# Kernel optimization log

Measured on AMD Instinct MI355X. Metric: run time of the kernel, lower is better.

## Reference

```python
import jax, jax.numpy as jnp
import numpy as np

B, D, F = 32768, 512, 512  # batch, input features, output features (num_feats)


def setup_inputs() -> dict:
    key = jax.random.key(0)
    kx, kw, ka, kb = jax.random.split(key, 4)
    x = jax.random.normal(kx, (B, D), dtype=jnp.float32)
    W = jax.random.normal(kw, (F, D), dtype=jnp.float32) / np.float32(np.sqrt(D))
    a = jax.random.normal(ka, (F,), dtype=jnp.float32)
    b = jax.random.normal(kb, (F,), dtype=jnp.float32)
    return {"x": x, "W": W, "a": a, "b": b}


def reference(x, W, a, b):
    # Vectorized form of the nested map_fn:
    # out[i, f] = tanh(b[f] + a[f] * dot(W[f, :], x[i, :]))
    z = jnp.einsum('bd,fd->bf', x, W)  # [B, F] GEMM replacing per-(sample,feature) dots
    return jnp.tanh(a * z + b)
```

## Files before the change

### kernel.cpp

```cpp
#include <hip/hip_runtime.h>
#include <hip/hip_bf16.h>
#include <math.h>


typedef short        bf16x8 __attribute__((ext_vector_type(8)));
typedef float        f32x4  __attribute__((ext_vector_type(4)));
typedef unsigned int u32x2  __attribute__((ext_vector_type(2)));

static constexpr int Mdim = 32768;
static constexpr int Kdim = 512;
static constexpr int Ndim = 512;

__device__ __forceinline__ unsigned cvt_pk_bf16(float a, float b) {
  unsigned r;
  asm("v_cvt_pk_bf16_f32 %0, %1, %2" : "=v"(r) : "v"(a), "v"(b));
  return r;
}

__device__ __forceinline__ void split4(f32x4 v, u32x2& hi, u32x2& lo) {
  unsigned h0 = cvt_pk_bf16(v[0], v[1]);
  unsigned h1 = cvt_pk_bf16(v[2], v[3]);
  float f0 = __uint_as_float(h0 << 16);
  float f1 = __uint_as_float(h0 & 0xFFFF0000u);
  float f2 = __uint_as_float(h1 << 16);
  float f3 = __uint_as_float(h1 & 0xFFFF0000u);
  lo[0] = cvt_pk_bf16(v[0] - f0, v[1] - f1);
  lo[1] = cvt_pk_bf16(v[2] - f2, v[3] - f3);
  hi[0] = h0; hi[1] = h1;
}

__device__ __forceinline__ float fast_tanh(float x) {
  float e = __expf(2.0f * x);
  return 1.0f - 2.0f * __builtin_amdgcn_rcpf(e + 1.0f);
}

__device__ __forceinline__ void glds16(const unsigned short* g, unsigned short* l) {
  __builtin_amdgcn_global_load_lds(
      (const __attribute__((address_space(1))) unsigned int*)g,
      (__attribute__((address_space(3))) unsigned int*)l, 16, 0, 0);
}

__global__ __launch_bounds__(256) void split_w(const float* __restrict__ Wm,
                                               unsigned short* __restrict__ whi,
                                               unsigned short* __restrict__ wlo) {
  const int idx = blockIdx.x * 256 + threadIdx.x;
  f32x4 v = *(const f32x4*)(Wm + (size_t)idx * 4);
  u32x2 h, l;
  split4(v, h, l);
  *(u32x2*)(whi + (size_t)idx * 4) = h;
  *(u32x2*)(wlo + (size_t)idx * 4) = l;
}

__global__ __launch_bounds__(512, 4) void gemm_ws(
    const float* __restrict__ X,
    const unsigned short* __restrict__ Whi, const unsigned short* __restrict__ Wlo,
    const float* __restrict__ avec, const float* __restrict__ bvec,
    float* __restrict__ out) {
  __shared__ unsigned short lds[4][128 * 64];

  const int bid = blockIdx.x;
  const int vid = (bid & 7) * 128 + (bid >> 3);
  const int nB  = vid & 3;
  const int mB  = vid >> 2;
  const int tid  = threadIdx.x;
  const int lane = tid & 63;
  const int wid  = tid >> 6;
  const int wm = wid >> 2, wn = wid & 3;

  f32x4 acc[4][2];
#pragma unroll
  for (int i = 0; i < 4; ++i)
#pragma unroll
    for (int j = 0; j < 2; ++j) acc[i][j] = {0.f, 0.f, 0.f, 0.f};

  const int srow  = tid >> 4;
  const int scol4 = tid & 15;
  const int kcol  = scol4 * 4;
  const int soff0 = kcol >> 3;
  const float* Xb = X + (size_t)mB * 128 * Kdim;

  const int rl = lane >> 3;
  const int ssl = (lane & 7) ^ rl;
  const int brow0 = nB * 128 + wid * 16 + rl;
  const int brow1 = brow0 + 8;
  const unsigned short* srcBhi0 = Whi + (size_t)brow0 * Kdim + ssl * 8;
  const unsigned short* srcBhi1 = Whi + (size_t)brow1 * Kdim + ssl * 8;
  const unsigned short* srcBlo0 = Wlo + (size_t)brow0 * Kdim + ssl * 8;
  const unsigned short* srcBlo1 = Wlo + (size_t)brow1 * Kdim + ssl * 8;
  unsigned short* dstB0 = &lds[0][(wid * 2 + 0) * 512];
  unsigned short* dstB1 = &lds[0][(wid * 2 + 1) * 512];
  const int planeSz = 128 * 64;

  f32x4 rA[4];
#pragma unroll
  for (int i = 0; i < 4; ++i)
    rA[i] = *(const f32x4*)(Xb + (size_t)(srow + 32 * i) * Kdim + kcol);

  for (int kt = 0; kt < Kdim / 64; ++kt) {
    const int kb = kt * 64;
    glds16(srcBhi0 + kb, dstB0 + 2 * planeSz);
    glds16(srcBhi1 + kb, dstB1 + 2 * planeSz);
    glds16(srcBlo0 + kb, dstB0 + 3 * planeSz);
    glds16(srcBlo1 + kb, dstB1 + 3 * planeSz);

#pragma unroll
    for (int i = 0; i < 4; ++i) {
      const int row = srow + 32 * i;
      const int off = row * 64 + ((soff0 ^ (row & 7)) << 3) + (kcol & 7);
      u32x2 h, l;
      split4(rA[i], h, l);
      *(u32x2*)&lds[0][off] = h;
      *(u32x2*)&lds[1][off] = l;
    }
    __syncthreads();

    if (kt != Kdim / 64 - 1) {
#pragma unroll
      for (int i = 0; i < 4; ++i)
        rA[i] = *(const f32x4*)(Xb + (size_t)(srow + 32 * i) * Kdim + kb + 64 + kcol);
    }

#pragma unroll
    for (int ks = 0; ks < 2; ++ks) {
      const int slotBase = ks * 4 + (lane >> 4);
      bf16x8 bh[2], bl[2];
#pragma unroll
      for (int ni = 0; ni < 2; ++ni) {
        const int row = wn * 32 + ni * 16 + (lane & 15);
        const int off = row * 64 + ((slotBase ^ (row & 7)) << 3);
        bh[ni] = *(const bf16x8*)&lds[2][off];
        bl[ni] = *(const bf16x8*)&lds[3][off];
      }
#pragma unroll
      for (int mi = 0; mi < 4; ++mi) {
        const int row = wm * 64 + mi * 16 + (lane & 15);
        const int off = row * 64 + ((slotBase ^ (row & 7)) << 3);
        bf16x8 ah = *(const bf16x8*)&lds[0][off];
        bf16x8 al = *(const bf16x8*)&lds[1][off];
#pragma unroll
        for (int ni = 0; ni < 2; ++ni) {
          acc[mi][ni] = __builtin_amdgcn_mfma_f32_16x16x32_bf16(ah, bh[ni], acc[mi][ni], 0, 0, 0);
          acc[mi][ni] = __builtin_amdgcn_mfma_f32_16x16x32_bf16(ah, bl[ni], acc[mi][ni], 0, 0, 0);
          acc[mi][ni] = __builtin_amdgcn_mfma_f32_16x16x32_bf16(al, bh[ni], acc[mi][ni], 0, 0, 0);
        }
      }
    }
    __syncthreads();
  }

  const int c  = lane & 15;
  const int rq = (lane >> 4) * 4;
#pragma unroll
  for (int ni = 0; ni < 2; ++ni) {
    const int gc = nB * 128 + wn * 32 + ni * 16 + c;
    const float aa = avec[gc];
    const float bb = bvec[gc];
#pragma unroll
    for (int mi = 0; mi < 4; ++mi) {
      const int gr = mB * 128 + wm * 64 + mi * 16 + rq;
      f32x4 v = acc[mi][ni];
#pragma unroll
      for (int j = 0; j < 4; ++j) {
        out[(size_t)(gr + j) * Ndim + gc] = fast_tanh(aa * v[j] + bb);
      }
    }
  }
}

__global__ __launch_bounds__(512, 4) void gemm_nows(
    const float* __restrict__ X, const float* __restrict__ Wm,
    const float* __restrict__ avec, const float* __restrict__ bvec,
    float* __restrict__ out) {
  __shared__ unsigned short lds[4][128 * 64];
  const int bid = blockIdx.x;
  const int nB  = bid & 3;
  const int mB  = bid >> 2;
  const int tid  = threadIdx.x;
  const int lane = tid & 63;
  const int wid  = tid >> 6;
  const int wm = wid >> 2, wn = wid & 3;

  f32x4 acc[4][2];
#pragma unroll
  for (int i = 0; i < 4; ++i)
#pragma unroll
    for (int j = 0; j < 2; ++j) acc[i][j] = {0.f, 0.f, 0.f, 0.f};

  const int srow  = tid >> 4;
  const int scol4 = tid & 15;
  const int kcol  = scol4 * 4;
  const int soff0 = kcol >> 3;
  const float* Xb = X  + (size_t)mB * 128 * Kdim;
  const float* Wb = Wm + (size_t)nB * 128 * Kdim;

  f32x4 rA[4], rB[4];
#pragma unroll
  for (int i = 0; i < 4; ++i) {
    const int row = srow + 32 * i;
    rA[i] = *(const f32x4*)(Xb + (size_t)row * Kdim + kcol);
    rB[i] = *(const f32x4*)(Wb + (size_t)row * Kdim + kcol);
  }

  for (int kt = 0; kt < Kdim / 64; ++kt) {
#pragma unroll
    for (int i = 0; i < 4; ++i) {
      const int row = srow + 32 * i;
      const int off = row * 64 + ((soff0 ^ (row & 7)) << 3) + (kcol & 7);
      u32x2 h, l;
      split4(rA[i], h, l);
      *(u32x2*)&lds[0][off] = h;
      *(u32x2*)&lds[1][off] = l;
      split4(rB[i], h, l);
      *(u32x2*)&lds[2][off] = h;
      *(u32x2*)&lds[3][off] = l;
    }
    __syncthreads();
    if (kt != Kdim / 64 - 1) {
      const int kbase = (kt + 1) * 64;
#pragma unroll
      for (int i = 0; i < 4; ++i) {
        const int row = srow + 32 * i;
        rA[i] = *(const f32x4*)(Xb + (size_t)row * Kdim + kbase + kcol);
        rB[i] = *(const f32x4*)(Wb + (size_t)row * Kdim + kbase + kcol);
      }
    }
#pragma unroll
    for (int ks = 0; ks < 2; ++ks) {
      const int slotBase = ks * 4 + (lane >> 4);
      bf16x8 bh[2], bl[2];
#pragma unroll
      for (int ni = 0; ni < 2; ++ni) {
        const int row = wn * 32 + ni * 16 + (lane & 15);
        const int off = row * 64 + ((slotBase ^ (row & 7)) << 3);
        bh[ni] = *(const bf16x8*)&lds[2][off];
        bl[ni] = *(const bf16x8*)&lds[3][off];
      }
#pragma unroll
      for (int mi = 0; mi < 4; ++mi) {
        const int row = wm * 64 + mi * 16 + (lane & 15);
        const int off = row * 64 + ((slotBase ^ (row & 7)) << 3);
        bf16x8 ah = *(const bf16x8*)&lds[0][off];
        bf16x8 al = *(const bf16x8*)&lds[1][off];
#pragma unroll
        for (int ni = 0; ni < 2; ++ni) {
          acc[mi][ni] = __builtin_amdgcn_mfma_f32_16x16x32_bf16(ah, bh[ni], acc[mi][ni], 0, 0, 0);
          acc[mi][ni] = __builtin_amdgcn_mfma_f32_16x16x32_bf16(ah, bl[ni], acc[mi][ni], 0, 0, 0);
          acc[mi][ni] = __builtin_amdgcn_mfma_f32_16x16x32_bf16(al, bh[ni], acc[mi][ni], 0, 0, 0);
        }
      }
    }
    __syncthreads();
  }

  const int c  = lane & 15;
  const int rq = (lane >> 4) * 4;
#pragma unroll
  for (int ni = 0; ni < 2; ++ni) {
    const int gc = nB * 128 + wn * 32 + ni * 16 + c;
    const float aa = avec[gc];
    const float bb = bvec[gc];
#pragma unroll
    for (int mi = 0; mi < 4; ++mi) {
      const int gr = mB * 128 + wm * 64 + mi * 16 + rq;
      f32x4 v = acc[mi][ni];
#pragma unroll
      for (int j = 0; j < 4; ++j) {
        out[(size_t)(gr + j) * Ndim + gc] = fast_tanh(aa * v[j] + bb);
      }
    }
  }
}

extern "C" void kernel_launch(void* const* d_in, const int* in_sizes, int n_in,
                              void* d_out, int out_size, void* d_ws, size_t ws_size,
                              hipStream_t stream) {
  const float* X  = (const float*)d_in[0];
  const float* Wm = (const float*)d_in[1];
  const float* av = (const float*)d_in[2];
  const float* bv = (const float*)d_in[3];
  float* out = (float*)d_out;

  const size_t wSplitBytes = (size_t)Ndim * Kdim * 2 * sizeof(unsigned short);
  if (ws_size >= wSplitBytes) {
    unsigned short* whi = (unsigned short*)d_ws;
    unsigned short* wlo = whi + (size_t)Ndim * Kdim;
    split_w<<<dim3(Ndim * Kdim / 4 / 256), dim3(256), 0, stream>>>(Wm, whi, wlo);
    gemm_ws<<<dim3((Mdim / 128) * (Ndim / 128)), dim3(512), 0, stream>>>(X, whi, wlo, av, bv, out);
  } else {
    gemm_nows<<<dim3((Mdim / 128) * (Ndim / 128)), dim3(512), 0, stream>>>(X, Wm, av, bv, out);
  }
}
```

Measured before the change: 158.0 us.

## Replace split-bf16 three-pass GEMM with single-pass fp16 MFMA and double-buffered LDS

Drops the hi/lo bf16 split, which needed three MFMAs per tile, and converts X and W to fp16 once, issuing a single fp16 MFMA per fragment pair. It also double-buffers LDS so the next K-tile's W (global_load_lds) and X loads overlap with the current tile's compute, leaving one barrier per iteration. This cuts MFMA work and LDS traffic by roughly three times. The cost is lower precision (fp16 with 10-bit mantissa instead of a ~16-bit split-bf16 product), which may or may not meet tolerance.

```diff
diff --git a/kernel.cpp b/kernel.cpp
--- a/kernel.cpp
+++ b/kernel.cpp
@@ -3,20 +3,158 @@
 #include <math.h>
 
 
-typedef short        bf16x8 __attribute__((ext_vector_type(8)));
-typedef float        f32x4  __attribute__((ext_vector_type(4)));
-typedef unsigned int u32x2  __attribute__((ext_vector_type(2)));
+typedef _Float16     f16x8 __attribute__((ext_vector_type(8)));
+typedef float        f32x4 __attribute__((ext_vector_type(4)));
+typedef unsigned int u32x2 __attribute__((ext_vector_type(2)));
 
 static constexpr int Mdim = 32768;
 static constexpr int Kdim = 512;
 static constexpr int Ndim = 512;
+
+__device__ __forceinline__ unsigned pk16(float a, float b) {
+  union { _Float16 h; unsigned short u; } ca, cb;
+  ca.h = (_Float16)a;
+  cb.h = (_Float16)b;
+  return (unsigned)ca.u | ((unsigned)cb.u << 16);
+}
+
+__device__ __forceinline__ float fast_tanh(float x) {
+  float e = __expf(2.0f * x);
+  return 1.0f - 2.0f * __builtin_amdgcn_rcpf(e + 1.0f);
+}
+
+__device__ __forceinline__ void glds16(const unsigned short* g, unsigned short* l) {
+  __builtin_amdgcn_global_load_lds(
+      (const __attribute__((address_space(1))) unsigned int*)g,
+      (__attribute__((address_space(3))) unsigned int*)l, 16, 0, 0);
+}
+
+__global__ __launch_bounds__(256) void conv_w(const float* __restrict__ Wm,
+                                              unsigned short* __restrict__ wh) {
+  const int idx = blockIdx.x * 256 + threadIdx.x;
+  f32x4 v = *(const f32x4*)(Wm + (size_t)idx * 4);
+  u32x2 p = { pk16(v[0], v[1]), pk16(v[2], v[3]) };
+  *(u32x2*)(wh + (size_t)idx * 4) = p;
+}
+
+__global__ __launch_bounds__(512, 4) void gemm_f16(
+    const float* __restrict__ X, const unsigned short* __restrict__ Wh,
+    const float* __restrict__ avec, const float* __restrict__ bvec,
+    float* __restrict__ out) {
+  __shared__ unsigned short lds[2][2][128 * 64];
+
+  const int bid = blockIdx.x;
+  const int vid = (bid & 7) * 128 + (bid >> 3);
+  const int nB  = vid & 3;
+  const int mB  = vid >> 2;
+  const int tid  = threadIdx.x;
+  const int lane = tid & 63;
+  const int wid  = tid >> 6;
+  const int wm = wid >> 2, wn = wid & 3;
+
+  f32x4 acc[4][2];
+#pragma unroll
+  for (int i = 0; i < 4; ++i)
+#pragma unroll
+    for (int j = 0; j < 2; ++j) acc[i][j] = {0.f, 0.f, 0.f, 0.f};
+
+  const int srow  = tid >> 4;
+  const int scol4 = tid & 15;
+  const int kcol  = scol4 * 4;
+  const int soff0 = kcol >> 3;
+  const float* Xb = X + (size_t)mB * 128 * Kdim;
+
+  const int rl  = lane >> 3;
+  const int ssl = (lane & 7) ^ rl;
+  const int brow0 = nB * 128 + wid * 16 + rl;
+  const unsigned short* sB0 = Wh + (size_t)brow0 * Kdim + ssl * 8;
+  const unsigned short* sB1 = Wh + (size_t)(brow0 + 8) * Kdim + ssl * 8;
+
+  glds16(sB0, &lds[0][1][(wid * 16) * 64]);
+  glds16(sB1, &lds[0][1][(wid * 16 + 8) * 64]);
+#pragma unroll
+  for (int i = 0; i < 4; ++i) {
+    const int row = srow + 32 * i;
+    f32x4 r = *(const f32x4*)(Xb + (size_t)row * Kdim + kcol);
+    const int off = row * 64 + ((soff0 ^ (row & 7)) << 3) + (kcol & 7);
+    u32x2 p = { pk16(r[0], r[1]), pk16(r[2], r[3]) };
+    *(u32x2*)&lds[0][0][off] = p;
+  }
+  __syncthreads();
+
+  int cur = 0;
+  for (int kt = 0; kt < Kdim / 64; ++kt) {
+    const int nxt = cur ^ 1;
+    f32x4 rA[4];
+    if (kt < Kdim / 64 - 1) {
+      const int kb = (kt + 1) * 64;
+      glds16(sB0 + kb, &lds[nxt][1][(wid * 16) * 64]);
+      glds16(sB1 + kb, &lds[nxt][1][(wid * 16 + 8) * 64]);
+#pragma unroll
+      for (int i = 0; i < 4; ++i)
+        rA[i] = *(const f32x4*)(Xb + (size_t)(srow + 32 * i) * Kdim + kb + kcol);
+    }
+
+#pragma unroll
+    for (int ks = 0; ks < 2; ++ks) {
+      const int slotBase = ks * 4 + (lane >> 4);
+      f16x8 bfr[2];
+#pragma unroll
+      for (int ni = 0; ni < 2; ++ni) {
+        const int row = wn * 32 + ni * 16 + (lane & 15);
+        const int off = row * 64 + ((slotBase ^ (row & 7)) << 3);
+        bfr[ni] = *(const f16x8*)&lds[cur][1][off];
+      }
+#pragma unroll
+      for (int mi = 0; mi < 4; ++mi) {
+        const int row = wm * 64 + mi * 16 + (lane & 15);
+        const int off = row * 64 + ((slotBase ^ (row & 7)) << 3);
+        f16x8 afr = *(const f16x8*)&lds[cur][0][off];
+#pragma unroll
+        for (int ni = 0; ni < 2; ++ni)
+          acc[mi][ni] = __builtin_amdgcn_mfma_f32_16x16x32_f16(afr, bfr[ni], acc[mi][ni], 0, 0, 0);
+      }
+    }
+
+    if (kt < Kdim / 64 - 1) {
+#pragma unroll
+      for (int i = 0; i < 4; ++i) {
+        const int row = srow + 32 * i;
+        const int off = row * 64 + ((soff0 ^ (row & 7)) << 3) + (kcol & 7);
+        u32x2 p = { pk16(rA[i][0], rA[i][1]), pk16(rA[i][2], rA[i][3]) };
+        *(u32x2*)&lds[nxt][0][off] = p;
+      }
+    }
+    __syncthreads();
+    cur = nxt;
+  }
+
+  const int c  = lane & 15;
+  const int rq = (lane >> 4) * 4;
+#pragma unroll
+  for (int ni = 0; ni < 2; ++ni) {
+    const int gc = nB * 128 + wn * 32 + ni * 16 + c;
+    const float aa = avec[gc];
+    const float bb = bvec[gc];
+#pragma unroll
+    for (int mi = 0; mi < 4; ++mi) {
+      const int gr = mB * 128 + wm * 64 + mi * 16 + rq;
+      f32x4 v = acc[mi][ni];
+#pragma unroll
+      for (int j = 0; j < 4; ++j) {
+        out[(size_t)(gr + j) * Ndim + gc] = fast_tanh(aa * v[j] + bb);
+      }
+    }
+  }
+}
+
+typedef short bf16x8 __attribute__((ext_vector_type(8)));
 
 __device__ __forceinline__ unsigned cvt_pk_bf16(float a, float b) {
   unsigned r;
   asm("v_cvt_pk_bf16_f32 %0, %1, %2" : "=v"(r) : "v"(a), "v"(b));
   return r;
 }
-
 __device__ __forceinline__ void split4(f32x4 v, u32x2& hi, u32x2& lo) {
   unsigned h0 = cvt_pk_bf16(v[0], v[1]);
   unsigned h1 = cvt_pk_bf16(v[2], v[3]);
@@ -27,144 +165,6 @@
   lo[0] = cvt_pk_bf16(v[0] - f0, v[1] - f1);
   lo[1] = cvt_pk_bf16(v[2] - f2, v[3] - f3);
   hi[0] = h0; hi[1] = h1;
-}
-
-__device__ __forceinline__ float fast_tanh(float x) {
-  float e = __expf(2.0f * x);
-  return 1.0f - 2.0f * __builtin_amdgcn_rcpf(e + 1.0f);
-}
-
-__device__ __forceinline__ void glds16(const unsigned short* g, unsigned short* l) {
-  __builtin_amdgcn_global_load_lds(
-      (const __attribute__((address_space(1))) unsigned int*)g,
-      (__attribute__((address_space(3))) unsigned int*)l, 16, 0, 0);
-}
-
-__global__ __launch_bounds__(256) void split_w(const float* __restrict__ Wm,
-                                               unsigned short* __restrict__ whi,
-                                               unsigned short* __restrict__ wlo) {
-  const int idx = blockIdx.x * 256 + threadIdx.x;
-  f32x4 v = *(const f32x4*)(Wm + (size_t)idx * 4);
-  u32x2 h, l;
-  split4(v, h, l);
-  *(u32x2*)(whi + (size_t)idx * 4) = h;
-  *(u32x2*)(wlo + (size_t)idx * 4) = l;
-}
-
-__global__ __launch_bounds__(512, 4) void gemm_ws(
-    const float* __restrict__ X,
-    const unsigned short* __restrict__ Whi, const unsigned short* __restrict__ Wlo,
-    const float* __restrict__ avec, const float* __restrict__ bvec,
-    float* __restrict__ out) {
-  __shared__ unsigned short lds[4][128 * 64];
-
-  const int bid = blockIdx.x;
-  const int vid = (bid & 7) * 128 + (bid >> 3);
-  const int nB  = vid & 3;
-  const int mB  = vid >> 2;
-  const int tid  = threadIdx.x;
-  const int lane = tid & 63;
-  const int wid  = tid >> 6;
-  const int wm = wid >> 2, wn = wid & 3;
-
-  f32x4 acc[4][2];
-#pragma unroll
-  for (int i = 0; i < 4; ++i)
-#pragma unroll
-    for (int j = 0; j < 2; ++j) acc[i][j] = {0.f, 0.f, 0.f, 0.f};
-
-  const int srow  = tid >> 4;
-  const int scol4 = tid & 15;
-  const int kcol  = scol4 * 4;
-  const int soff0 = kcol >> 3;
-  const float* Xb = X + (size_t)mB * 128 * Kdim;
-
-  const int rl = lane >> 3;
-  const int ssl = (lane & 7) ^ rl;
-  const int brow0 = nB * 128 + wid * 16 + rl;
-  const int brow1 = brow0 + 8;
-  const unsigned short* srcBhi0 = Whi + (size_t)brow0 * Kdim + ssl * 8;
-  const unsigned short* srcBhi1 = Whi + (size_t)brow1 * Kdim + ssl * 8;
-  const unsigned short* srcBlo0 = Wlo + (size_t)brow0 * Kdim + ssl * 8;
-  const unsigned short* srcBlo1 = Wlo + (size_t)brow1 * Kdim + ssl * 8;
-  unsigned short* dstB0 = &lds[0][(wid * 2 + 0) * 512];
-  unsigned short* dstB1 = &lds[0][(wid * 2 + 1) * 512];
-  const int planeSz = 128 * 64;
-
-  f32x4 rA[4];
-#pragma unroll
-  for (int i = 0; i < 4; ++i)
-    rA[i] = *(const f32x4*)(Xb + (size_t)(srow + 32 * i) * Kdim + kcol);
-
-  for (int kt = 0; kt < Kdim / 64; ++kt) {
-    const int kb = kt * 64;
-    glds16(srcBhi0 + kb, dstB0 + 2 * planeSz);
-    glds16(srcBhi1 + kb, dstB1 + 2 * planeSz);
-    glds16(srcBlo0 + kb, dstB0 + 3 * planeSz);
-    glds16(srcBlo1 + kb, dstB1 + 3 * planeSz);
-
-#pragma unroll
-    for (int i = 0; i < 4; ++i) {
-      const int row = srow + 32 * i;
-      const int off = row * 64 + ((soff0 ^ (row & 7)) << 3) + (kcol & 7);
-      u32x2 h, l;
-      split4(rA[i], h, l);
-      *(u32x2*)&lds[0][off] = h;
-      *(u32x2*)&lds[1][off] = l;
-    }
-    __syncthreads();
-
-    if (kt != Kdim / 64 - 1) {
-#pragma unroll
-      for (int i = 0; i < 4; ++i)
-        rA[i] = *(const f32x4*)(Xb + (size_t)(srow + 32 * i) * Kdim + kb + 64 + kcol);
-    }
-
-#pragma unroll
-    for (int ks = 0; ks < 2; ++ks) {
-      const int slotBase = ks * 4 + (lane >> 4);
-      bf16x8 bh[2], bl[2];
-#pragma unroll
-      for (int ni = 0; ni < 2; ++ni) {
-        const int row = wn * 32 + ni * 16 + (lane & 15);
-        const int off = row * 64 + ((slotBase ^ (row & 7)) << 3);
-        bh[ni] = *(const bf16x8*)&lds[2][off];
-        bl[ni] = *(const bf16x8*)&lds[3][off];
-      }
-#pragma unroll
-      for (int mi = 0; mi < 4; ++mi) {
-        const int row = wm * 64 + mi * 16 + (lane & 15);
-        const int off = row * 64 + ((slotBase ^ (row & 7)) << 3);
-        bf16x8 ah = *(const bf16x8*)&lds[0][off];
-        bf16x8 al = *(const bf16x8*)&lds[1][off];
-#pragma unroll
-        for (int ni = 0; ni < 2; ++ni) {
-          acc[mi][ni] = __builtin_amdgcn_mfma_f32_16x16x32_bf16(ah, bh[ni], acc[mi][ni], 0, 0, 0);
-          acc[mi][ni] = __builtin_amdgcn_mfma_f32_16x16x32_bf16(ah, bl[ni], acc[mi][ni], 0, 0, 0);
-          acc[mi][ni] = __builtin_amdgcn_mfma_f32_16x16x32_bf16(al, bh[ni], acc[mi][ni], 0, 0, 0);
-        }
-      }
-    }
-    __syncthreads();
-  }
-
-  const int c  = lane & 15;
-  const int rq = (lane >> 4) * 4;
-#pragma unroll
-  for (int ni = 0; ni < 2; ++ni) {
-    const int gc = nB * 128 + wn * 32 + ni * 16 + c;
-    const float aa = avec[gc];
-    const float bb = bvec[gc];
-#pragma unroll
-    for (int mi = 0; mi < 4; ++mi) {
-      const int gr = mB * 128 + wm * 64 + mi * 16 + rq;
-      f32x4 v = acc[mi][ni];
-#pragma unroll
-      for (int j = 0; j < 4; ++j) {
-        out[(size_t)(gr + j) * Ndim + gc] = fast_tanh(aa * v[j] + bb);
-      }
-    }
-  }
 }
 
 __global__ __launch_bounds__(512, 4) void gemm_nows(
@@ -200,7 +200,6 @@
     rA[i] = *(const f32x4*)(Xb + (size_t)row * Kdim + kcol);
     rB[i] = *(const f32x4*)(Wb + (size_t)row * Kdim + kcol);
   }
-
   for (int kt = 0; kt < Kdim / 64; ++kt) {
 #pragma unroll
     for (int i = 0; i < 4; ++i) {
@@ -251,7 +250,6 @@
     }
     __syncthreads();
   }
-
   const int c  = lane & 15;
   const int rq = (lane >> 4) * 4;
 #pragma unroll
@@ -280,12 +278,11 @@
   const float* bv = (const float*)d_in[3];
   float* out = (float*)d_out;
 
-  const size_t wSplitBytes = (size_t)Ndim * Kdim * 2 * sizeof(unsigned short);
-  if (ws_size >= wSplitBytes) {
-    unsigned short* whi = (unsigned short*)d_ws;
-    unsigned short* wlo = whi + (size_t)Ndim * Kdim;
-    split_w<<<dim3(Ndim * Kdim / 4 / 256), dim3(256), 0, stream>>>(Wm, whi, wlo);
-    gemm_ws<<<dim3((Mdim / 128) * (Ndim / 128)), dim3(512), 0, stream>>>(X, whi, wlo, av, bv, out);
+  const size_t wBytes = (size_t)Ndim * Kdim * sizeof(unsigned short);
+  if (ws_size >= wBytes) {
+    unsigned short* wh = (unsigned short*)d_ws;
+    conv_w<<<dim3(Ndim * Kdim / 4 / 256), dim3(256), 0, stream>>>(Wm, wh);
+    gemm_f16<<<dim3((Mdim / 128) * (Ndim / 128)), dim3(512), 0, stream>>>(X, wh, av, bv, out);
   } else {
     gemm_nows<<<dim3((Mdim / 128) * (Ndim / 128)), dim3(512), 0, stream>>>(X, Wm, av, bv, out);
   }
```

New measurement: 146.3 us. 7.4% less time.
